# Kernel optimization log

Hardware: AMD Instinct MI355X
Metric: run time of the kernel (lower is better)

Reference implementation:

```python
import jax, jax.numpy as jnp
import numpy as np

D = 512; E = 8; TOPK = 2; F = 2048; H = 4
SF_LEVELS = 4; SF_BASE = 4.0; LN_EPS = 1e-5


def _ln(h, s, b):
    mu = jnp.mean(h, axis=-1, keepdims=True)
    var = jnp.mean((h - mu) ** 2, axis=-1, keepdims=True)
    return (h - mu) / jnp.sqrt(var + LN_EPS) * s + b


def setup_inputs() -> dict:
    key = jax.random.key(0)
    ks = jax.random.split(key, 16)
    sc = 0.02
    inp = {
        "x": jax.random.normal(ks[0], (4, 1024, D), jnp.float32),
        "gate_w": jax.random.normal(ks[1], (D, E), jnp.float32) * sc,
        "gate_b": jnp.zeros((E,), jnp.float32),
        "ln1_s": jnp.ones((E, D), jnp.float32),
        "ln1_b": jnp.zeros((E, D), jnp.float32),
        "ln2_s": jnp.ones((E, D), jnp.float32),
        "ln2_b": jnp.zeros((E, D), jnp.float32),
        "wq": jax.random.normal(ks[2], (E, D, D), jnp.float32) * sc,
        "wk": jax.random.normal(ks[3], (E, D, D), jnp.float32) * sc,
        "wv": jax.random.normal(ks[4], (E, D, D), jnp.float32) * sc,
        "wo": jax.random.normal(ks[5], (E, D, D), jnp.float32) * sc,
        "bq": jnp.zeros((E, D), jnp.float32),
        "bk": jnp.zeros((E, D), jnp.float32),
        "bv": jnp.zeros((E, D), jnp.float32),
        "bo": jnp.zeros((E, D), jnp.float32),
        "w1": jax.random.normal(ks[6], (E, D, F), jnp.float32) * sc,
        "b1": jnp.zeros((E, F), jnp.float32),
        "w2": jax.random.normal(ks[7], (E, F, D), jnp.float32) * sc,
        "b2": jnp.zeros((E, D), jnp.float32),
    }
    return inp


def reference(x, gate_w, gate_b, ln1_s, ln1_b, ln2_s, ln2_b, wq, wk, wv, wo, bq, bk, bv, bo, w1, b1, w2, b2):
    B, S, d = x.shape
    dh = d // H
    # --- SpikingRouter ---
    logits = x @ gate_w + gate_b                       # [B,S,E]
    _, idx = jax.lax.top_k(logits, TOPK)               # [B,S,k]
    in_topk = jnp.sum(jax.nn.one_hot(idx, E, dtype=logits.dtype), axis=-2) > 0
    routing_in = jnp.where(in_topk, jax.nn.relu(logits), 0.0)
    # Scale-and-Fire neuron: multi-level threshold quantization
    mem = routing_in
    rw = jnp.zeros_like(mem)
    for lvl in range(SF_LEVELS):
        thr = SF_BASE / (2.0 ** lvl)
        spk = (mem >= thr).astype(mem.dtype)
        rw = rw + spk * thr
        mem = mem - spk * thr
    # --- all experts (SFormerBlock, post-norm transformer block) ---
    def block(p):
        l1s, l1b, l2s, l2b, Wq, Wk, Wv, Wo, Bq, Bk, Bv, Bo, W1, B1, W2, B2 = p
        q = (x @ Wq + Bq).reshape(B, S, H, dh)
        k = (x @ Wk + Bk).reshape(B, S, H, dh)
        v = (x @ Wv + Bv).reshape(B, S, H, dh)
        scores = jnp.einsum('bqhd,bkhd->bhqk', q, k) / jnp.sqrt(jnp.asarray(dh, x.dtype))
        att = jax.nn.softmax(scores, axis=-1)
        o = jnp.einsum('bhqk,bkhd->bqhd', att, v).reshape(B, S, d) @ Wo + Bo
        h = _ln(x + o, l1s, l1b)
        f = jax.nn.relu(h @ W1 + B1) @ W2 + B2
        return _ln(h + f, l2s, l2b)

    expert_outs = jax.vmap(block)((ln1_s, ln1_b, ln2_s, ln2_b, wq, wk, wv, wo, bq, bk, bv, bo, w1, b1, w2, b2))  # [E,B,S,D]
    final = jnp.einsum('ebsd,bse->bsd', expert_outs, rw)
    return final, logits
```

## Files before the change

kernel.cpp:

```cpp
#include <hip/hip_runtime.h>
#include <hip/hip_bf16.h>
#include <stdint.h>

using u16 = unsigned short;
typedef float floatx4 __attribute__((ext_vector_type(4)));
typedef __bf16 bfv8 __attribute__((ext_vector_type(8)));

#define AS1 __attribute__((address_space(1)))
#define AS3 __attribute__((address_space(3)))

__device__ __forceinline__ u16 f2bf_bits(float f) {
    __hip_bfloat16 h = __float2bfloat16(f);
    u16 u;
    __builtin_memcpy(&u, &h, 2);
    return u;
}
__device__ __forceinline__ float bf_bits2f(u16 u) {
    __hip_bfloat16 h;
    __builtin_memcpy(&h, &u, 2);
    return __bfloat162float(h);
}
__device__ __forceinline__ void gload_lds16(const void* g, void* l) {
    __builtin_amdgcn_global_load_lds((AS1 void*)(uintptr_t)g, (AS3 void*)l, 16, 0, 0);
}

__device__ __forceinline__ void stage64(const u16* __restrict__ Abase, long lda, const long* arow,
                                        const u16* __restrict__ Bb, long ldb, int k0, int tid,
                                        u16* Ad, u16* Bd) {
    #pragma unroll
    for (int j = 0; j < 4; ++j) {
        const int q   = j * 256 + tid;
        const int row = q >> 3;
        const int cg  = (q & 7) ^ (row & 7);
        gload_lds16(Abase + arow[j] * lda + k0 + cg * 8, Ad + q * 8);
        gload_lds16(Bb + (long)row * ldb + k0 + cg * 8, Bd + q * 8);
    }
}
__device__ __forceinline__ void stage_one(const u16* __restrict__ base, long ld, int tid, u16* dst) {
    #pragma unroll
    for (int j = 0; j < 4; ++j) {
        const int q   = j * 256 + tid;
        const int row = q >> 3;
        const int cg  = (q & 7) ^ (row & 7);
        gload_lds16(base + (long)row * ld + cg * 8, dst + q * 8);
    }
}
__device__ __forceinline__ void compute64(const u16* Ab, const u16* Bb, int wy, int wx,
                                          int quad, int mrow, floatx4 acc[4][4]) {
    #pragma unroll
    for (int kk = 0; kk < 2; ++kk) {
        bfv8 af[4], bf[4];
        #pragma unroll
        for (int mi = 0; mi < 4; mi++) {
            const int r = wy * 64 + mi * 16 + mrow;
            const int slot = (kk * 4 + quad) ^ (r & 7);
            af[mi] = *(const bfv8*)&Ab[r * 64 + slot * 8];
        }
        #pragma unroll
        for (int ni = 0; ni < 4; ni++) {
            const int r = wx * 64 + ni * 16 + mrow;
            const int slot = (kk * 4 + quad) ^ (r & 7);
            bf[ni] = *(const bfv8*)&Bb[r * 64 + slot * 8];
        }
        #pragma unroll
        for (int mi = 0; mi < 4; mi++)
            #pragma unroll
            for (int ni = 0; ni < 4; ni++)
                acc[mi][ni] = __builtin_amdgcn_mfma_f32_16x16x32_bf16(af[mi], bf[ni], acc[mi][ni], 0, 0, 0);
    }
}
__device__ __forceinline__ void computeQK(const u16* Kb, const bfv8 qf[2][4], int wy,
                                          int quad, int mrow, floatx4 acc[4][4]) {
    #pragma unroll
    for (int kk = 0; kk < 2; ++kk) {
        bfv8 af[4];
        #pragma unroll
        for (int mi = 0; mi < 4; mi++) {
            const int r = wy * 64 + mi * 16 + mrow;
            const int slot = (kk * 4 + quad) ^ (r & 7);
            af[mi] = *(const bfv8*)&Kb[r * 64 + slot * 8];
        }
        #pragma unroll
        for (int mi = 0; mi < 4; mi++)
            #pragma unroll
            for (int ni = 0; ni < 4; ni++)
                acc[mi][ni] = __builtin_amdgcn_mfma_f32_16x16x32_bf16(af[mi], qf[kk][ni], acc[mi][ni], 0, 0, 0);
    }
}

__global__ void transpose_all_kernel(const float* __restrict__ wq, const float* __restrict__ wk,
                                     const float* __restrict__ wv, const float* __restrict__ wo,
                                     const float* __restrict__ w1, const float* __restrict__ w2,
                                     u16* __restrict__ WB) {
    __shared__ float tile[32][33];
    const int bid = blockIdx.x;
    const float* s; u16* d; int R, C, c0, r0;
    if (bid < 8192) {
        int x = bid & 15, y = (bid >> 4) & 15, z = bid >> 8;
        s = (z < 8 ? wq : z < 16 ? wk : z < 24 ? wv : wo) + (long)(z & 7) * 262144;
        d = WB + (long)z * 262144;
        R = 512; C = 512; c0 = x * 32; r0 = y * 32;
    } else if (bid < 16384) {
        int idx = bid - 8192;
        int x = idx & 63, y = (idx >> 6) & 15, z = idx >> 10;
        s = w1 + (long)z * 1048576;
        d = WB + 8388608 + (long)z * 1048576;
        R = 512; C = 2048; c0 = x * 32; r0 = y * 32;
    } else {
        int idx = bid - 16384;
        int x = idx & 15, y = (idx >> 4) & 63, z = idx >> 10;
        s = w2 + (long)z * 1048576;
        d = WB + 16777216 + (long)z * 1048576;
        R = 2048; C = 512; c0 = x * 32; r0 = y * 32;
    }
    int tx = threadIdx.x, ty = threadIdx.y;
    #pragma unroll
    for (int i = 0; i < 4; i++)
        tile[ty + 8*i][tx] = s[(long)(r0 + ty + 8*i) * C + c0 + tx];
    __syncthreads();
    #pragma unroll
    for (int i = 0; i < 4; i++)
        d[(long)(c0 + ty + 8*i) * R + r0 + tx] = f2bf_bits(tile[tx][ty + 8*i]);
}

__global__ __launch_bounds__(512)
void router_cast_kernel(const float* __restrict__ x, const float* __restrict__ gw,
                        const float* __restrict__ gb, float* __restrict__ rw,
                        float* __restrict__ logits_out, u16* __restrict__ xb,
                        const float* __restrict__ bq, const float* __restrict__ bk,
                        const float* __restrict__ bvv, float* __restrict__ pb) {
    if (blockIdx.x >= 4096) {
        int j = (blockIdx.x - 4096) * 512 + threadIdx.x;
        const float* s = j < 4096 ? bq : (j < 8192 ? bk : bvv);
        pb[j] = s[j & 4095];
        return;
    }
    int row = blockIdx.x;
    int w = threadIdx.x >> 6;
    int lane = threadIdx.x & 63;
    const float* xr = x + (long)row * 512;
    float sum = 0.f;
    #pragma unroll
    for (int i = 0; i < 8; i++) {
        int d = lane + 64 * i;
        float v = xr[d];
        sum += v * gw[d * 8 + w];
        if (i == w) xb[(long)row * 512 + d] = f2bf_bits(v);
    }
    #pragma unroll
    for (int o = 32; o; o >>= 1) sum += __shfl_down(sum, o, 64);
    __shared__ float lg[8];
    if (lane == 0) lg[w] = sum + gb[w];
    __syncthreads();
    if (threadIdx.x == 0) {
        float l[8];
        #pragma unroll
        for (int e = 0; e < 8; e++) l[e] = lg[e];
        int i1 = 0;
        for (int e = 1; e < 8; e++) if (l[e] > l[i1]) i1 = e;
        int i2 = -1;
        for (int e = 0; e < 8; e++) { if (e == i1) continue; if (i2 < 0 || l[e] > l[i2]) i2 = e; }
        for (int e = 0; e < 8; e++) {
            float v = (e == i1 || e == i2) ? (l[e] > 0.f ? l[e] : 0.f) : 0.f;
            float r = 0.f, mem = v;
            #pragma unroll
            for (int lvl = 0; lvl < 4; lvl++) {
                float thr = 4.0f / (float)(1 << lvl);
                if (mem >= thr) { r += thr; mem -= thr; }
            }
            rw[(long)row * 8 + e] = r;
            logits_out[(long)row * 8 + e] = l[e];
        }
    }
}

__global__ __launch_bounds__(256)
void build_lists_kernel(const float* __restrict__ rw, int* __restrict__ prix,
                        int* __restrict__ act, int* __restrict__ smap,
                        int* __restrict__ tmap, int* __restrict__ tt, int* __restrict__ pt) {
    int b = blockIdx.x;
    int t = threadIdx.x, wv = t >> 6, lane = t & 63;
    __shared__ int wsum[4];
    __shared__ int base_sh;
    if (t == 0) base_sh = 0;
    __syncthreads();
    for (int e = 0; e < 8; e++) {
        int r0 = b * 1024 + t * 4;
        int f[4], c = 0;
        #pragma unroll
        for (int i = 0; i < 4; i++) {
            f[i] = (rw[(long)(r0 + i) * 8 + e] != 0.f) ? 1 : 0;
            c += f[i];
        }
        int incl = c;
        #pragma unroll
        for (int o = 1; o < 64; o <<= 1) {
            int n = __shfl_up(incl, o, 64);
            if (lane >= o) incl += n;
        }
        if (lane == 63) wsum[wv] = incl;
        __syncthreads();
        int woff = 0;
        #pragma unroll
        for (int k = 0; k < 4; k++) if (k < wv) woff += wsum[k];
        int tot = wsum[0] + wsum[1] + wsum[2] + wsum[3];
        int excl = incl - c + woff;
        int base = base_sh;
        int slot = excl;
        #pragma unroll
        for (int i = 0; i < 4; i++) {
            int r = r0 + i;
            if (f[i]) {
                int ps = base + slot;
                prix[b * 3072 + ps] = r;
                act[b * 3072 + ps] = 1;
                smap[(long)r * 8 + e] = ps;
                slot++;
            } else {
                smap[(long)r * 8 + e] = -1;
            }
        }
        int pad = (tot + 127) & ~127;
        for (int s = tot + t; s < pad; s += 256) {
            prix[b * 3072 + base + s] = b * 1024;
            act[b * 3072 + base + s] = 0;
        }
        for (int k = t; k < (pad >> 7); k += 256)
            tmap[b * 32 + (base >> 7) + k] = e;
        __syncthreads();
        if (t == 0) base_sh = base + pad;
        __syncthreads();
    }
    if (t == 0) {
        tt[b] = base_sh >> 7;
        pt[b] = base_sh;
    }
}

__global__ __launch_bounds__(256)
void gemm_kv_kernel(const u16* __restrict__ A,
                    const u16* __restrict__ Wkv,
                    u16* __restrict__ CK, u16* __restrict__ CV,
                    const float* __restrict__ biasKV) {
    __shared__ __align__(16) u16 As[2][128 * 64];
    __shared__ __align__(16) u16 Bs[2][128 * 64];
    const int z = blockIdx.z;
    const u16* Bb = Wkv + (long)z * 262144 + (long)blockIdx.x * 128 * 512;

    const int tid = threadIdx.x;
    const int w = tid >> 6, lane = tid & 63;
    const int wy = w >> 1, wx = w & 1;
    const int quad = lane >> 4, mrow = lane & 15;

    long arow[4];
    #pragma unroll
    for (int j = 0; j < 4; ++j) arow[j] = (long)blockIdx.y * 128 + ((j * 256 + tid) >> 3);

    floatx4 acc[4][4];
    #pragma unroll
    for (int i = 0; i < 4; i++)
        #pragma unroll
        for (int j = 0; j < 4; j++)
            acc[i][j] = floatx4{0.f, 0.f, 0.f, 0.f};

    stage64(A, 512, arow, Bb, 512, 0, tid, As[0], Bs[0]);
    for (int it = 0; it < 8; ++it) {
        const int cur = it & 1;
        __syncthreads();
        if (it + 1 < 8)
            stage64(A, 512, arow, Bb, 512, (it + 1) << 6, tid, As[1 - cur], Bs[1 - cur]);
        compute64(As[cur], Bs[cur], wy, wx, quad, mrow, acc);
    }

    const float* biasb = biasKV + (long)z * 512 + blockIdx.x * 128;
    if (z >= 8) {
        u16* Cb = CV + (long)(z - 8) * 2097152;
        #pragma unroll
        for (int ni = 0; ni < 4; ni++) {
            const int colt = wx * 64 + ni * 16 + mrow;
            const int n = blockIdx.x * 128 + colt;
            float bv = biasb[colt];
            #pragma unroll
            for (int mi = 0; mi < 4; mi++) {
                const int m = blockIdx.y * 128 + wy * 64 + mi * 16 + quad * 4;
                long addr = ((long)(((m >> 10) << 2) + (n >> 7)) * 128 + (n & 127)) * 1024 + (m & 1023);
                ushort4 st;
                st.x = f2bf_bits(acc[mi][ni][0] + bv);
                st.y = f2bf_bits(acc[mi][ni][1] + bv);
                st.z = f2bf_bits(acc[mi][ni][2] + bv);
                st.w = f2bf_bits(acc[mi][ni][3] + bv);
                *(ushort4*)(Cb + addr) = st;
            }
        }
    } else {
        u16* Cb = CK + (long)z * 2097152 + (long)blockIdx.y * 128 * 512 + blockIdx.x * 128;
        #pragma unroll
        for (int ni = 0; ni < 4; ni++) {
            const int col = wx * 64 + ni * 16 + mrow;
            float bv = biasb[col];
            #pragma unroll
            for (int mi = 0; mi < 4; mi++) {
                #pragma unroll
                for (int r = 0; r < 4; r++) {
                    const int row = wy * 64 + mi * 16 + quad * 4 + r;
                    Cb[(long)row * 512 + col] = f2bf_bits(acc[mi][ni][r] + bv);
                }
            }
        }
    }
}

__global__ __launch_bounds__(256)
void gemm_qp_kernel(const u16* __restrict__ XB, const u16* __restrict__ Wq,
                    u16* __restrict__ QP, const float* __restrict__ biasQ,
                    const int* __restrict__ tmap, const int* __restrict__ tt,
                    const int* __restrict__ prix) {
    const int b = blockIdx.y / 24, tile = blockIdx.y % 24;
    if (tile >= tt[b]) return;
    const int e = tmap[b * 32 + tile];
    __shared__ __align__(16) u16 As[2][128 * 64];
    __shared__ __align__(16) u16 Bs[2][128 * 64];
    const long rbase = (long)b * 3072 + tile * 128;
    const u16* Bb = Wq + (long)e * 262144 + (long)blockIdx.x * 128 * 512;

    const int tid = threadIdx.x;
    const int w = tid >> 6, lane = tid & 63;
    const int wy = w >> 1, wx = w & 1;
    const int quad = lane >> 4, mrow = lane & 15;

    long arow[4];
    #pragma unroll
    for (int j = 0; j < 4; ++j)
        arow[j] = (long)prix[b * 3072 + tile * 128 + ((j * 256 + tid) >> 3)];

    floatx4 acc[4][4];
    #pragma unroll
    for (int i = 0; i < 4; i++)
        #pragma unroll
        for (int j = 0; j < 4; j++)
            acc[i][j] = floatx4{0.f, 0.f, 0.f, 0.f};

    stage64(XB, 512, arow, Bb, 512, 0, tid, As[0], Bs[0]);
    for (int it = 0; it < 8; ++it) {
        const int cur = it & 1;
        __syncthreads();
        if (it + 1 < 8)
            stage64(XB, 512, arow, Bb, 512, (it + 1) << 6, tid, As[1 - cur], Bs[1 - cur]);
        compute64(As[cur], Bs[cur], wy, wx, quad, mrow, acc);
    }

    u16* Cb = QP + rbase * 512 + blockIdx.x * 128;
    const float* biasb = biasQ + blockIdx.x * 128;
    #pragma unroll
    for (int ni = 0; ni < 4; ni++) {
        const int col = wx * 64 + ni * 16 + mrow;
        float bv = biasb[col];
        #pragma unroll
        for (int mi = 0; mi < 4; mi++) {
            #pragma unroll
            for (int r = 0; r < 4; r++) {
                const int row = wy * 64 + mi * 16 + quad * 4 + r;
                Cb[(long)row * 512 + col] = f2bf_bits(acc[mi][ni][r] + bv);
            }
        }
    }
}

__global__ __launch_bounds__(256, 2)
void attn_fused_kernel(const u16* __restrict__ QP, const u16* __restrict__ Km,
                       const u16* __restrict__ VT, u16* __restrict__ OC,
                       const int* __restrict__ tmap, const int* __restrict__ tt, float alpha) {
    const int tile = blockIdx.x;
    const int bh = blockIdx.y;
    const int b = bh >> 2, h = bh & 3;
    if (tile >= tt[b]) return;
    const int e = tmap[b * 32 + tile];

    __shared__ __align__(16) u16 Bs[2][128 * 64];
    __shared__ __align__(16) u16 Ps[2][128 * 64];
    __shared__ float rs_sh[2][128];

    const int tid = threadIdx.x;
    const int w = tid >> 6, lane = tid & 63;
    const int wy = w >> 1, wx = w & 1;
    const int quad = lane >> 4, mrow = lane & 15;

    const u16* Qbase = QP + ((long)b * 3072 + tile * 128) * 512 + h * 128;
    const u16* Kbase = Km + ((long)e * 4096 + b * 1024) * 512 + h * 128;
    const u16* Vbase = VT + ((long)e * 16 + bh) * 131072;

    stage_one(Qbase, 512, tid, Ps[0]);
    stage_one(Qbase + 64, 512, tid, Ps[1]);
    __syncthreads();
    bfv8 qf[2][2][4];
    #pragma unroll
    for (int c = 0; c < 2; c++)
        #pragma unroll
        for (int kk = 0; kk < 2; kk++)
            #pragma unroll
            for (int ni = 0; ni < 4; ni++) {
                const int r = wx * 64 + ni * 16 + mrow;
                const int slot = (kk * 4 + quad) ^ (r & 7);
                qf[c][kk][ni] = *(const bfv8*)&Ps[c][r * 64 + slot * 8];
            }

    floatx4 acc_o[4][4];
    float rsum[4];
    #pragma unroll
    for (int i = 0; i < 4; i++) {
        rsum[i] = 0.f;
        #pragma unroll
        for (int j = 0; j < 4; j++) acc_o[i][j] = floatx4{0.f, 0.f, 0.f, 0.f};
    }

    for (int kt = 0; kt < 8; ++kt) {
        __syncthreads();
        stage_one(Kbase + (long)kt * 128 * 512,      512, tid, Bs[0]);
        stage_one(Kbase + (long)kt * 128 * 512 + 64, 512, tid, Bs[1]);
        __syncthreads();

        floatx4 acc_s[4][4];
        #pragma unroll
        for (int i = 0; i < 4; i++)
            #pragma unroll
            for (int j = 0; j < 4; j++) acc_s[i][j] = floatx4{0.f, 0.f, 0.f, 0.f};
        computeQK(Bs[0], qf[0], wy, quad, mrow, acc_s);
        computeQK(Bs[1], qf[1], wy, quad, mrow, acc_s);

        #pragma unroll
        for (int mi = 0; mi < 4; mi++)
            #pragma unroll
            for (int ni = 0; ni < 4; ni++)
                #pragma unroll
                for (int r = 0; r < 4; r++) {
                    float p = __expf(acc_s[mi][ni][r] * alpha);
                    acc_s[mi][ni][r] = p;
                    rsum[ni] += p;
                }

        __syncthreads();
        stage_one(Vbase + kt * 128,      1024, tid, Bs[0]);
        stage_one(Vbase + kt * 128 + 64, 1024, tid, Bs[1]);
        u16* Pw = Ps[wy];
        #pragma unroll
        for (int mi = 0; mi < 4; mi++) {
            const int sb = mi * 2 + (quad >> 1);
            #pragma unroll
            for (int ni = 0; ni < 4; ni++) {
                const int q = wx * 64 + ni * 16 + mrow;
                u16* pr = Pw + q * 64 + (sb ^ (q & 7)) * 8 + (quad & 1) * 4;
                #pragma unroll
                for (int r = 0; r < 4; r += 2) {
                    uint32_t pk = (uint32_t)f2bf_bits(acc_s[mi][ni][r]) |
                                  ((uint32_t)f2bf_bits(acc_s[mi][ni][r + 1]) << 16);
                    *(uint32_t*)(pr + r) = pk;
                }
            }
        }
        __syncthreads();
        compute64(Bs[0], Ps[0], wy, wx, quad, mrow, acc_o);
        compute64(Bs[1], Ps[1], wy, wx, quad, mrow, acc_o);
    }

    #pragma unroll
    for (int ni = 0; ni < 4; ni++) {
        float v = rsum[ni];
        v += __shfl_xor(v, 16, 64);
        v += __shfl_xor(v, 32, 64);
        if (quad == 0) rs_sh[wy][wx * 64 + ni * 16 + mrow] = v;
    }
    __syncthreads();
    u16* Cb = OC + ((long)b * 3072 + tile * 128) * 512 + h * 128;
    #pragma unroll
    for (int ni = 0; ni < 4; ni++) {
        const int q = wx * 64 + ni * 16 + mrow;
        const float inv = 1.f / (rs_sh[0][q] + rs_sh[1][q]);
        #pragma unroll
        for (int mi = 0; mi < 4; mi++) {
            ushort4 st;
            st.x = f2bf_bits(acc_o[mi][ni][0] * inv);
            st.y = f2bf_bits(acc_o[mi][ni][1] * inv);
            st.z = f2bf_bits(acc_o[mi][ni][2] * inv);
            st.w = f2bf_bits(acc_o[mi][ni][3] * inv);
            *(ushort4*)(Cb + (long)q * 512 + wy * 64 + mi * 16 + quad * 4) = st;
        }
    }
}

template<bool RELU>
__global__ __launch_bounds__(256)
void gemm_packed_kernel(const u16* __restrict__ A, int lda,
                        const u16* __restrict__ B, int ldb, long sBe,
                        u16* __restrict__ C, int ldc,
                        const float* __restrict__ bias, long sBiasE,
                        const int* __restrict__ tmap, const int* __restrict__ tt, int K) {
    const int b = blockIdx.y / 24, tile = blockIdx.y % 24;
    if (tile >= tt[b]) return;
    const int e = tmap[b * 32 + tile];
    __shared__ __align__(16) u16 As[2][128 * 64];
    __shared__ __align__(16) u16 Bs[2][128 * 64];
    const long rbase = (long)b * 3072 + tile * 128;
    const u16* Ab = A + rbase * lda;
    const u16* Bb = B + (long)e * sBe + (long)blockIdx.x * 128 * ldb;

    const int tid = threadIdx.x;
    const int w = tid >> 6, lane = tid & 63;
    const int wy = w >> 1, wx = w & 1;
    const int quad = lane >> 4, mrow = lane & 15;

    long arow[4];
    #pragma unroll
    for (int j = 0; j < 4; ++j) arow[j] = (j * 256 + tid) >> 3;

    floatx4 acc[4][4];
    #pragma unroll
    for (int i = 0; i < 4; i++)
        #pragma unroll
        for (int j = 0; j < 4; j++)
            acc[i][j] = floatx4{0.f, 0.f, 0.f, 0.f};

    const int nk = K >> 6;
    stage64(Ab, lda, arow, Bb, ldb, 0, tid, As[0], Bs[0]);
    for (int it = 0; it < nk; ++it) {
        const int cur = it & 1;
        __syncthreads();
        if (it + 1 < nk)
            stage64(Ab, lda, arow, Bb, ldb, (it + 1) << 6, tid, As[1 - cur], Bs[1 - cur]);
        compute64(As[cur], Bs[cur], wy, wx, quad, mrow, acc);
    }

    u16* Cb = C + rbase * ldc + (long)blockIdx.x * 128;
    const float* biasb = bias + (long)e * sBiasE + blockIdx.x * 128;
    #pragma unroll
    for (int ni = 0; ni < 4; ni++) {
        const int col = wx * 64 + ni * 16 + mrow;
        float bv = biasb[col];
        #pragma unroll
        for (int mi = 0; mi < 4; mi++) {
            #pragma unroll
            for (int r = 0; r < 4; r++) {
                const int row = wy * 64 + mi * 16 + quad * 4 + r;
                float v = acc[mi][ni][r] + bv;
                if (RELU) v = fmaxf(v, 0.f);
                Cb[(long)row * ldc + col] = f2bf_bits(v);
            }
        }
    }
}

__global__ __launch_bounds__(256)
void gemm_ffn2_half_kernel(const u16* __restrict__ MID, const u16* __restrict__ W2T,
                           float* __restrict__ P0, float* __restrict__ P1,
                           const int* __restrict__ tmap, const int* __restrict__ tt) {
    const int b = blockIdx.y / 24, tile = blockIdx.y % 24;
    if (tile >= tt[b]) return;
    const int e = tmap[b * 32 + tile];
    __shared__ __align__(16) u16 As[2][128 * 64];
    __shared__ __align__(16) u16 Bs[2][128 * 64];
    const long rbase = (long)b * 3072 + tile * 128;
    const int koff = blockIdx.z * 1024;
    const u16* Ab = MID + rbase * 2048 + koff;
    const u16* Bb = W2T + (long)e * 1048576 + (long)blockIdx.x * 128 * 2048 + koff;

    const int tid = threadIdx.x;
    const int w = tid >> 6, lane = tid & 63;
    const int wy = w >> 1, wx = w & 1;
    const int quad = lane >> 4, mrow = lane & 15;

    long arow[4];
    #pragma unroll
    for (int j = 0; j < 4; ++j) arow[j] = (j * 256 + tid) >> 3;

    floatx4 acc[4][4];
    #pragma unroll
    for (int i = 0; i < 4; i++)
        #pragma unroll
        for (int j = 0; j < 4; j++)
            acc[i][j] = floatx4{0.f, 0.f, 0.f, 0.f};

    stage64(Ab, 2048, arow, Bb, 2048, 0, tid, As[0], Bs[0]);
    for (int it = 0; it < 16; ++it) {
        const int cur = it & 1;
        __syncthreads();
        if (it + 1 < 16)
            stage64(Ab, 2048, arow, Bb, 2048, (it + 1) << 6, tid, As[1 - cur], Bs[1 - cur]);
        compute64(As[cur], Bs[cur], wy, wx, quad, mrow, acc);
    }

    float* Cb = (blockIdx.z ? P1 : P0) + rbase * 512 + (long)blockIdx.x * 128;
    #pragma unroll
    for (int ni = 0; ni < 4; ni++) {
        const int col = wx * 64 + ni * 16 + mrow;
        #pragma unroll
        for (int mi = 0; mi < 4; mi++) {
            #pragma unroll
            for (int r = 0; r < 4; r++) {
                const int row = wy * 64 + mi * 16 + quad * 4 + r;
                Cb[(long)row * 512 + col] = acc[mi][ni][r];
            }
        }
    }
}

__global__ __launch_bounds__(128)
void ln1_kernel(const float* __restrict__ x, const u16* __restrict__ tc,
                const int* __restrict__ prix, const int* __restrict__ act,
                const int* __restrict__ tmap, const int* __restrict__ pt,
                const float* __restrict__ s_all, const float* __restrict__ b_all,
                u16* __restrict__ hb) {
    int blk = blockIdx.x;
    int b = blk / 3072, pslot = blk % 3072;
    if (pslot >= pt[b]) return;
    long row = (long)b * 3072 + pslot;
    int tid = threadIdx.x, w = tid >> 6, lane = tid & 63;
    if (!act[row]) {
        *(ushort4*)(hb + row * 512 + tid * 4) = make_ushort4(0, 0, 0, 0);
        return;
    }
    int r = prix[row];
    int e = tmap[b * 32 + (pslot >> 7)];
    float4 xv = *(const float4*)(x + (long)r * 512 + tid * 4);
    ushort4 tu = *(const ushort4*)(tc + row * 512 + tid * 4);
    float v[4] = {xv.x + bf_bits2f(tu.x), xv.y + bf_bits2f(tu.y),
                  xv.z + bf_bits2f(tu.z), xv.w + bf_bits2f(tu.w)};
    float sum = v[0] + v[1] + v[2] + v[3];
    #pragma unroll
    for (int o = 32; o; o >>= 1) sum += __shfl_down(sum, o, 64);
    __shared__ float sh[4];
    if (lane == 0) sh[w] = sum;
    __syncthreads();
    float mu = (sh[0] + sh[1]) * (1.f / 512.f);
    float sq = 0.f;
    #pragma unroll
    for (int j = 0; j < 4; j++) { float d = v[j] - mu; sq += d * d; }
    #pragma unroll
    for (int o = 32; o; o >>= 1) sq += __shfl_down(sq, o, 64);
    if (lane == 0) sh[2 + w] = sq;
    __syncthreads();
    float inv = 1.f / sqrtf((sh[2] + sh[3]) * (1.f / 512.f) + 1e-5f);
    float4 sv = *(const float4*)(s_all + e * 512 + tid * 4);
    float4 bv = *(const float4*)(b_all + e * 512 + tid * 4);
    ushort4 ub;
    ub.x = f2bf_bits((v[0] - mu) * inv * sv.x + bv.x);
    ub.y = f2bf_bits((v[1] - mu) * inv * sv.y + bv.y);
    ub.z = f2bf_bits((v[2] - mu) * inv * sv.z + bv.z);
    ub.w = f2bf_bits((v[3] - mu) * inv * sv.w + bv.w);
    *(ushort4*)(hb + row * 512 + tid * 4) = ub;
}

__global__ __launch_bounds__(128)
void ln2acc_kernel(const u16* __restrict__ hb, const float* __restrict__ p0,
                   const float* __restrict__ p1, const float* __restrict__ b2,
                   const float* __restrict__ s_all, const float* __restrict__ b_all,
                   const float* __restrict__ rw, const int* __restrict__ smap,
                   float* __restrict__ out) {
    long r = blockIdx.x;
    int b = (int)(r >> 10);
    int tid = threadIdx.x, w = tid >> 6, lane = tid & 63;
    __shared__ float sh[4];
    float4 acc = make_float4(0.f, 0.f, 0.f, 0.f);
    for (int e = 0; e < 8; e++) {
        int ps = smap[r * 8 + e];
        if (ps >= 0) {
            float wgt = rw[r * 8 + e];
            long row = (long)b * 3072 + ps;
            ushort4 hu = *(const ushort4*)(hb + row * 512 + tid * 4);
            float4 f0 = *(const float4*)(p0 + row * 512 + tid * 4);
            float4 f1 = *(const float4*)(p1 + row * 512 + tid * 4);
            float4 bb = *(const float4*)(b2 + (long)e * 512 + tid * 4);
            float v[4] = {bf_bits2f(hu.x) + f0.x + f1.x + bb.x,
                          bf_bits2f(hu.y) + f0.y + f1.y + bb.y,
                          bf_bits2f(hu.z) + f0.z + f1.z + bb.z,
                          bf_bits2f(hu.w) + f0.w + f1.w + bb.w};
            float sum = v[0] + v[1] + v[2] + v[3];
            #pragma unroll
            for (int o = 32; o; o >>= 1) sum += __shfl_down(sum, o, 64);
            if (lane == 0) sh[w] = sum;
            __syncthreads();
            float mu = (sh[0] + sh[1]) * (1.f / 512.f);
            float sq = 0.f;
            #pragma unroll
            for (int j = 0; j < 4; j++) { float d = v[j] - mu; sq += d * d; }
            #pragma unroll
            for (int o = 32; o; o >>= 1) sq += __shfl_down(sq, o, 64);
            if (lane == 0) sh[2 + w] = sq;
            __syncthreads();
            float inv = 1.f / sqrtf((sh[2] + sh[3]) * (1.f / 512.f) + 1e-5f);
            float4 sv = *(const float4*)(s_all + e * 512 + tid * 4);
            float4 bv = *(const float4*)(b_all + e * 512 + tid * 4);
            acc.x += wgt * ((v[0] - mu) * inv * sv.x + bv.x);
            acc.y += wgt * ((v[1] - mu) * inv * sv.y + bv.y);
            acc.z += wgt * ((v[2] - mu) * inv * sv.z + bv.z);
            acc.w += wgt * ((v[3] - mu) * inv * sv.w + bv.w);
            __syncthreads();
        }
    }
    *(float4*)(out + r * 512 + tid * 4) = acc;
}

static const size_t WB_B   = 0;
static const size_t RW_B   = 50331648;
static const size_t PB_B   = 50462720;
static const size_t TT_B   = 50511872;
static const size_t PT_B   = 50511888;
static const size_t TMAP_B = 50511904;
static const size_t PRIX_B = 50512416;
static const size_t ACT_B  = 50561568;
static const size_t SMAP_B = 50610720;
static const size_t XB_B   = 50741792;
static const size_t Q8_B   = 54936096;
static const size_t K8_B   = 88490528;
static const size_t VT_B   = 122044960;
static const size_t S_B    = 155599392;
static const size_t OC_B   = Q8_B;
static const size_t TC_B   = K8_B;
static const size_t HB_B   = Q8_B;
static const size_t MID_B  = S_B;
static const size_t FP0_B  = VT_B;
static const size_t FP1_B  = 205931040;

extern "C" void kernel_launch(void* const* d_in, const int* in_sizes, int n_in,
                              void* d_out, int out_size, void* d_ws, size_t ws_size,
                              hipStream_t stream) {
    const float* x      = (const float*)d_in[0];
    const float* gate_w = (const float*)d_in[1];
    const float* gate_b = (const float*)d_in[2];
    const float* ln1_s  = (const float*)d_in[3];
    const float* ln1_b  = (const float*)d_in[4];
    const float* ln2_s  = (const float*)d_in[5];
    const float* ln2_b  = (const float*)d_in[6];
    const float* wq = (const float*)d_in[7];
    const float* wk = (const float*)d_in[8];
    const float* wv = (const float*)d_in[9];
    const float* wo = (const float*)d_in[10];
    const float* bo = (const float*)d_in[14];
    const float* w1 = (const float*)d_in[15];
    const float* b1 = (const float*)d_in[16];
    const float* w2 = (const float*)d_in[17];
    const float* b2 = (const float*)d_in[18];
    float* out = (float*)d_out;

    char* ws = (char*)d_ws;
    u16*   WB   = (u16*)(ws + WB_B);
    float* RW   = (float*)(ws + RW_B);
    float* PB   = (float*)(ws + PB_B);
    int*   TT   = (int*)(ws + TT_B);
    int*   PT   = (int*)(ws + PT_B);
    int*   TMAP = (int*)(ws + TMAP_B);
    int*   PRIX = (int*)(ws + PRIX_B);
    int*   ACT  = (int*)(ws + ACT_B);
    int*   SMAP = (int*)(ws + SMAP_B);
    u16*   XB   = (u16*)(ws + XB_B);
    u16*   QP   = (u16*)(ws + Q8_B);
    u16*   K8   = (u16*)(ws + K8_B);
    u16*   VT8  = (u16*)(ws + VT_B);
    u16*   OC   = (u16*)(ws + OC_B);
    u16*   TC   = (u16*)(ws + TC_B);
    u16*   HB   = (u16*)(ws + HB_B);
    u16*   MID  = (u16*)(ws + MID_B);
    float* FP0  = (float*)(ws + FP0_B);
    float* FP1  = (float*)(ws + FP1_B);

    transpose_all_kernel<<<dim3(24576), dim3(32,8), 0, stream>>>(wq, wk, wv, wo, w1, w2, WB);
    router_cast_kernel<<<4120, 512, 0, stream>>>(x, gate_w, gate_b, RW, out + 2097152, XB,
                                                 (const float*)d_in[11], (const float*)d_in[12],
                                                 (const float*)d_in[13], PB);
    build_lists_kernel<<<4, 256, 0, stream>>>(RW, PRIX, ACT, SMAP, TMAP, TT, PT);

    const float isq = 0.08838834764831845f;

    gemm_kv_kernel<<<dim3(4,32,16), 256, 0, stream>>>(XB, WB + 2097152, K8, VT8, PB + 4096);
    gemm_qp_kernel<<<dim3(4,96), 256, 0, stream>>>(XB, WB, QP, PB, TMAP, TT, PRIX);

    attn_fused_kernel<<<dim3(24, 16), 256, 0, stream>>>(QP, K8, VT8, OC, TMAP, TT, isq);

    gemm_packed_kernel<false><<<dim3(4,96), 256, 0, stream>>>(
        OC, 512, WB + 6291456, 512, 262144, TC, 512, bo, 512, TMAP, TT, 512);
    ln1_kernel<<<12288, 128, 0, stream>>>(x, TC, PRIX, ACT, TMAP, PT, ln1_s, ln1_b, HB);
    gemm_packed_kernel<true><<<dim3(16,96), 256, 0, stream>>>(
        HB, 512, WB + 8388608, 512, 1048576, MID, 2048, b1, 2048, TMAP, TT, 512);
    gemm_ffn2_half_kernel<<<dim3(4,96,2), 256, 0, stream>>>(
        MID, WB + 16777216, FP0, FP1, TMAP, TT);
    ln2acc_kernel<<<4096, 128, 0, stream>>>(HB, FP0, FP1, b2, ln2_s, ln2_b, RW, SMAP, out);
}
```

Before: 418.4 us.

## Fuse Q projection GEMM into attention kernel prologue

Removes the separate gemm_qp kernel and computes each head's 128-row Q tile inside the attention kernel, reading gathered X rows and the transposed Wq slice straight from global memory into MFMA fragments. The bias-added bf16 result goes into the swizzled LDS buffer the attention loop already reads from. This drops one kernel launch and the QP write and read round trip. In exchange the projection is done without LDS staging or double buffering, using uncoalesced per-lane global loads.

```diff
diff --git a/kernel.cpp b/kernel.cpp
--- a/kernel.cpp
+++ b/kernel.cpp
@@ -310,66 +310,13 @@
     }
 }
 
-__global__ __launch_bounds__(256)
-void gemm_qp_kernel(const u16* __restrict__ XB, const u16* __restrict__ Wq,
-                    u16* __restrict__ QP, const float* __restrict__ biasQ,
-                    const int* __restrict__ tmap, const int* __restrict__ tt,
-                    const int* __restrict__ prix) {
-    const int b = blockIdx.y / 24, tile = blockIdx.y % 24;
-    if (tile >= tt[b]) return;
-    const int e = tmap[b * 32 + tile];
-    __shared__ __align__(16) u16 As[2][128 * 64];
-    __shared__ __align__(16) u16 Bs[2][128 * 64];
-    const long rbase = (long)b * 3072 + tile * 128;
-    const u16* Bb = Wq + (long)e * 262144 + (long)blockIdx.x * 128 * 512;
-
-    const int tid = threadIdx.x;
-    const int w = tid >> 6, lane = tid & 63;
-    const int wy = w >> 1, wx = w & 1;
-    const int quad = lane >> 4, mrow = lane & 15;
-
-    long arow[4];
-    #pragma unroll
-    for (int j = 0; j < 4; ++j)
-        arow[j] = (long)prix[b * 3072 + tile * 128 + ((j * 256 + tid) >> 3)];
-
-    floatx4 acc[4][4];
-    #pragma unroll
-    for (int i = 0; i < 4; i++)
-        #pragma unroll
-        for (int j = 0; j < 4; j++)
-            acc[i][j] = floatx4{0.f, 0.f, 0.f, 0.f};
-
-    stage64(XB, 512, arow, Bb, 512, 0, tid, As[0], Bs[0]);
-    for (int it = 0; it < 8; ++it) {
-        const int cur = it & 1;
-        __syncthreads();
-        if (it + 1 < 8)
-            stage64(XB, 512, arow, Bb, 512, (it + 1) << 6, tid, As[1 - cur], Bs[1 - cur]);
-        compute64(As[cur], Bs[cur], wy, wx, quad, mrow, acc);
-    }
-
-    u16* Cb = QP + rbase * 512 + blockIdx.x * 128;
-    const float* biasb = biasQ + blockIdx.x * 128;
-    #pragma unroll
-    for (int ni = 0; ni < 4; ni++) {
-        const int col = wx * 64 + ni * 16 + mrow;
-        float bv = biasb[col];
-        #pragma unroll
-        for (int mi = 0; mi < 4; mi++) {
-            #pragma unroll
-            for (int r = 0; r < 4; r++) {
-                const int row = wy * 64 + mi * 16 + quad * 4 + r;
-                Cb[(long)row * 512 + col] = f2bf_bits(acc[mi][ni][r] + bv);
-            }
-        }
-    }
-}
-
 __global__ __launch_bounds__(256, 2)
-void attn_fused_kernel(const u16* __restrict__ QP, const u16* __restrict__ Km,
-                       const u16* __restrict__ VT, u16* __restrict__ OC,
-                       const int* __restrict__ tmap, const int* __restrict__ tt, float alpha) {
+void attn_fused_kernel(const u16* __restrict__ XB, const u16* __restrict__ WqT,
+                       const float* __restrict__ biasQ,
+                       const u16* __restrict__ Km, const u16* __restrict__ VT,
+                       u16* __restrict__ OC,
+                       const int* __restrict__ tmap, const int* __restrict__ tt,
+                       const int* __restrict__ prix, float alpha) {
     const int tile = blockIdx.x;
     const int bh = blockIdx.y;
     const int b = bh >> 2, h = bh & 3;
@@ -385,12 +332,57 @@
     const int wy = w >> 1, wx = w & 1;
     const int quad = lane >> 4, mrow = lane & 15;
 
-    const u16* Qbase = QP + ((long)b * 3072 + tile * 128) * 512 + h * 128;
     const u16* Kbase = Km + ((long)e * 4096 + b * 1024) * 512 + h * 128;
     const u16* Vbase = VT + ((long)e * 16 + bh) * 131072;
 
-    stage_one(Qbase, 512, tid, Ps[0]);
-    stage_one(Qbase + 64, 512, tid, Ps[1]);
+    const u16* Aq = WqT + (long)e * 262144 + (long)(h * 128) * 512;
+    long qrow[4];
+    #pragma unroll
+    for (int ni = 0; ni < 4; ++ni)
+        qrow[ni] = (long)prix[b * 3072 + tile * 128 + wx * 64 + ni * 16 + mrow];
+
+    floatx4 acc_q[4][4];
+    #pragma unroll
+    for (int i = 0; i < 4; i++)
+        #pragma unroll
+        for (int j = 0; j < 4; j++) acc_q[i][j] = floatx4{0.f, 0.f, 0.f, 0.f};
+
+    #pragma unroll
+    for (int ks = 0; ks < 16; ++ks) {
+        bfv8 af[4], bf[4];
+        #pragma unroll
+        for (int mi = 0; mi < 4; ++mi)
+            af[mi] = *(const bfv8*)(Aq + (long)(wy * 64 + mi * 16 + mrow) * 512 + ks * 32 + quad * 8);
+        #pragma unroll
+        for (int ni = 0; ni < 4; ++ni)
+            bf[ni] = *(const bfv8*)(XB + qrow[ni] * 512 + ks * 32 + quad * 8);
+        #pragma unroll
+        for (int mi = 0; mi < 4; ++mi)
+            #pragma unroll
+            for (int ni = 0; ni < 4; ++ni)
+                acc_q[mi][ni] = __builtin_amdgcn_mfma_f32_16x16x32_bf16(af[mi], bf[ni], acc_q[mi][ni], 0, 0, 0);
+    }
+
+    {
+        const float* bqp = biasQ + e * 512 + h * 128 + wy * 64;
+        u16* Pw = Ps[wy];
+        #pragma unroll
+        for (int mi = 0; mi < 4; mi++) {
+            const float4 bqv = *(const float4*)(bqp + mi * 16 + quad * 4);
+            const int sb = mi * 2 + (quad >> 1);
+            #pragma unroll
+            for (int ni = 0; ni < 4; ni++) {
+                const int q = wx * 64 + ni * 16 + mrow;
+                u16* pr = Pw + q * 64 + (sb ^ (q & 7)) * 8 + (quad & 1) * 4;
+                uint32_t pk0 = (uint32_t)f2bf_bits(acc_q[mi][ni][0] + bqv.x) |
+                               ((uint32_t)f2bf_bits(acc_q[mi][ni][1] + bqv.y) << 16);
+                uint32_t pk1 = (uint32_t)f2bf_bits(acc_q[mi][ni][2] + bqv.z) |
+                               ((uint32_t)f2bf_bits(acc_q[mi][ni][3] + bqv.w) << 16);
+                *(uint32_t*)pr = pk0;
+                *(uint32_t*)(pr + 2) = pk1;
+            }
+        }
+    }
     __syncthreads();
     bfv8 qf[2][2][4];
     #pragma unroll
@@ -751,7 +743,6 @@
     int*   ACT  = (int*)(ws + ACT_B);
     int*   SMAP = (int*)(ws + SMAP_B);
     u16*   XB   = (u16*)(ws + XB_B);
-    u16*   QP   = (u16*)(ws + Q8_B);
     u16*   K8   = (u16*)(ws + K8_B);
     u16*   VT8  = (u16*)(ws + VT_B);
     u16*   OC   = (u16*)(ws + OC_B);
@@ -770,9 +761,9 @@
     const float isq = 0.08838834764831845f;
 
     gemm_kv_kernel<<<dim3(4,32,16), 256, 0, stream>>>(XB, WB + 2097152, K8, VT8, PB + 4096);
-    gemm_qp_kernel<<<dim3(4,96), 256, 0, stream>>>(XB, WB, QP, PB, TMAP, TT, PRIX);
-
-    attn_fused_kernel<<<dim3(24, 16), 256, 0, stream>>>(QP, K8, VT8, OC, TMAP, TT, isq);
+
+    attn_fused_kernel<<<dim3(24, 16), 256, 0, stream>>>(
+        XB, WB, PB, K8, VT8, OC, TMAP, TT, PRIX, isq);
 
     gemm_packed_kernel<false><<<dim3(4,96), 256, 0, stream>>>(
         OC, 512, WB + 6291456, 512, 262144, TC, 512, bo, 512, TMAP, TT, 512);
```

New measurement: 453.0 us. +8.3%, slower.
